# Kernel optimization log

Hardware: AMD Instinct MI355X
Metric: run time of the kernel (lower is better)

Reference implementation:

```python
import jax, jax.numpy as jnp
import numpy as np

N_NODES = 100000
N_EDGES = 1600000
N_GRAPHS = 1000
IN_DIM, HID, OUT = 100, 128, 2


def setup_inputs() -> dict:
    key = jax.random.key(0)
    ks = jax.random.split(key, 9)
    x = jax.random.normal(ks[0], (N_NODES, IN_DIM), dtype=jnp.float32)
    edge_index = jax.random.randint(ks[1], (2, N_EDGES), 0, N_NODES, dtype=jnp.int64 if jax.config.jax_enable_x64 else jnp.int32)
    batch = jnp.sort(jax.random.randint(ks[2], (N_NODES,), 0, N_GRAPHS))
    W1 = jax.random.normal(ks[3], (IN_DIM, HID), dtype=jnp.float32) / np.sqrt(IN_DIM)
    b1 = jax.random.normal(ks[4], (HID,), dtype=jnp.float32) * 0.01
    W2 = jax.random.normal(ks[5], (HID, HID), dtype=jnp.float32) / np.sqrt(HID)
    b2 = jax.random.normal(ks[6], (HID,), dtype=jnp.float32) * 0.01
    Wfc = jax.random.normal(ks[7], (HID, OUT), dtype=jnp.float32) / np.sqrt(HID)
    bfc = jax.random.normal(ks[8], (OUT,), dtype=jnp.float32) * 0.01
    return {"x": x, "edge_index": edge_index, "batch": batch, "num_graphs": N_GRAPHS,
            "W1": W1, "b1": b1, "W2": W2, "b2": b2, "Wfc": Wfc, "bfc": bfc}


def reference(x, edge_index, batch, num_graphs, W1, b1, W2, b2, Wfc, bfc):
    n = x.shape[0]
    loop = jnp.arange(n, dtype=edge_index.dtype)
    # GCNConv default: add self loops, then symmetric normalization
    src = jnp.concatenate([edge_index[0], loop])  # [E+N]
    dst = jnp.concatenate([edge_index[1], loop])
    deg = jax.ops.segment_sum(jnp.ones_like(dst, dtype=x.dtype), dst, num_segments=n)  # in-degree incl self-loop
    dinv = jnp.where(deg > 0, jax.lax.rsqrt(deg), 0.0)
    norm = (dinv[src] * dinv[dst])[:, None]  # [E+N,1]

    def gcn_conv(h, W, b):
        h = h @ W                                # transform-first (small feat dim)
        msg = h[src] * norm                      # gather + scale  [E+N, F]
        agg = jax.ops.segment_sum(msg, dst, num_segments=n)  # scatter-add
        return agg + b

    h = jax.nn.relu(gcn_conv(x, W1, b1))
    h = jax.nn.relu(gcn_conv(h, W2, b2))

    # global_mean_pool over graphs
    sums = jax.ops.segment_sum(h, batch, num_segments=num_graphs)
    cnts = jax.ops.segment_sum(jnp.ones((n,), dtype=h.dtype), batch, num_segments=num_graphs)
    pooled = sums / jnp.maximum(cnts, 1.0)[:, None]
    # dropout is identity at inference
    return pooled @ Wfc + bfc
```

## Files before the change

kernel.cpp:

```cpp
#include <hip/hip_runtime.h>


#define GCN_GRAPHS 1000
#define CSR_CAP 64
#define BUCKET_CAP 4608
#define BIN_TILE 8192
#define POOL_CHUNKS 4

typedef short bf16x8 __attribute__((ext_vector_type(8)));
typedef float f32x4 __attribute__((ext_vector_type(4)));
typedef float f32x2 __attribute__((ext_vector_type(2)));

__device__ __forceinline__ unsigned short f2bf(float x) {
  unsigned u = __float_as_uint(x);
  return (unsigned short)((u + 0x7fff + ((u >> 16) & 1)) >> 16);
}
__device__ __forceinline__ f32x2 fp8x2_f32(unsigned short u) {
  return __builtin_amdgcn_cvt_pk_f32_fp8((int)(unsigned)u, false);
}
__device__ __forceinline__ unsigned char f32_fp8(float v) {
  return (unsigned char)(__builtin_amdgcn_cvt_pk_fp8_f32(v, v, 0, false) & 0xff);
}

__global__ __launch_bounds__(256) void setup_kernel(
    const float* __restrict__ W1, const float* __restrict__ W2,
    unsigned short* __restrict__ Wf1, unsigned short* __restrict__ Wf2,
    int* __restrict__ gcursor, int nbk, const int* __restrict__ batch,
    const float* __restrict__ bfc, float* __restrict__ out,
    float* __restrict__ invcnt, int* __restrict__ gstart,
    unsigned char* __restrict__ hs1, unsigned char* __restrict__ hs2,
    int N, int G) {
  int t = blockIdx.x * 256 + threadIdx.x;
  if (t < nbk) gcursor[t] = t * BUCKET_CAP;
  if (t < 32) {
    ((unsigned*)(hs1 + ((size_t)N << 7)))[t] = 0u;
    ((unsigned*)(hs2 + ((size_t)N << 7)))[t] = 0u;
  }
  if (t <= G) {
    int lo = 0, hi = N;
    while (lo < hi) { int mid = (lo + hi) >> 1; if (batch[mid] < t) lo = mid + 1; else hi = mid; }
    gstart[t] = lo;
    if (t < G) {
      int s = lo;
      hi = N;
      while (lo < hi) { int mid = (lo + hi) >> 1; if (batch[mid] < t + 1) lo = mid + 1; else hi = mid; }
      int cnt = lo - s;
      invcnt[t] = (cnt > 0) ? 1.f / (float)cnt : 0.f;
      out[2 * t + 0] = bfc[0];
      out[2 * t + 1] = bfc[1];
    }
  }
  for (int o = t; o < 16384; o += 4096) {
    int L = (o >> 3) & 63, j = o & 7;
    int tnq = o >> 9;
    int kq = tnq >> 3, tn = tnq & 7;
    int k = kq * 32 + (L >> 4) * 8 + j;
    int n = tn * 16 + (L & 15);
    Wf1[o] = (k < 100) ? f2bf(W1[k * 128 + n]) : (unsigned short)0;
    Wf2[o] = f2bf(W2[k * 128 + n]);
  }
}

__global__ __launch_bounds__(512) void bin_kernel(
    const int* __restrict__ src, const int* __restrict__ dst,
    int* __restrict__ gcursor, int* __restrict__ bucketbuf, int E, int nbk) {
  __shared__ int hist[512];
  __shared__ int off[512];
  __shared__ int gbase[512];
  __shared__ int lcur[512];
  __shared__ int wsum[8];
  __shared__ int stage[BIN_TILE];
  __shared__ int gofs[BIN_TILE];
  const int tid = threadIdx.x;
  const int lane = tid & 63, wv = tid >> 6;
  const int tile0 = blockIdx.x * BIN_TILE;
  int cnt = E - tile0;
  if (cnt > BIN_TILE) cnt = BIN_TILE;

  hist[tid] = 0;
  __syncthreads();
  for (int i = tid; i < cnt; i += 512) {
    int b = dst[tile0 + i] >> 8;
    atomicAdd(&hist[b], 1);
  }
  __syncthreads();
  int v = hist[tid];
  int inc = v;
#pragma unroll
  for (int s = 1; s < 64; s <<= 1) {
    int u = __shfl_up(inc, s);
    if (lane >= s) inc += u;
  }
  if (lane == 63) wsum[wv] = inc;
  __syncthreads();
  if (wv == 0 && lane < 8) {
    int p = wsum[lane];
#pragma unroll
    for (int s = 1; s < 8; s <<= 1) {
      int u = __shfl_up(p, s);
      if (lane >= s) p += u;
    }
    wsum[lane] = p;
  }
  __syncthreads();
  int excl = (wv ? wsum[wv - 1] : 0) + inc - v;
  off[tid] = excl;
  if (tid < nbk && v > 0)
    gbase[tid] = atomicAdd(&gcursor[tid], v);
  lcur[tid] = 0;
  __syncthreads();
  for (int i = tid; i < cnt; i += 512) {
    int d = dst[tile0 + i];
    int s = src[tile0 + i];
    int b = d >> 8;
    int r = atomicAdd(&lcur[b], 1);
    int pos = off[b] + r;
    stage[pos] = s | ((d & 255) << 17);
    int ga = gbase[b] + r;
    gofs[pos] = (ga < (b + 1) * BUCKET_CAP) ? ga : -1;
  }
  __syncthreads();
  for (int j = tid; j < cnt; j += 512) {
    int a = gofs[j];
    if (a >= 0) bucketbuf[a] = stage[j];
  }
}

__global__ __launch_bounds__(256) void build_kernel(
    const int* __restrict__ gcursor, const int* __restrict__ bucketbuf,
    int* __restrict__ csr, int* __restrict__ deg, int N) {
  __shared__ int lcnt[256];
  __shared__ int lcsr[256 * CSR_CAP];
  const int tid = threadIdx.x;
  const int b = blockIdx.x;
  const int base = b * BUCKET_CAP;
  int cnt = gcursor[b] - base;
  if (cnt > BUCKET_CAP) cnt = BUCKET_CAP;
  lcnt[tid] = 0;
  __syncthreads();
  for (int i = tid; i < cnt; i += 256) {
    int val = bucketbuf[base + i];
    int ld = val >> 17, s = val & 0x1FFFF;
    int r = atomicAdd(&lcnt[ld], 1);
    if (r < CSR_CAP) lcsr[ld * CSR_CAP + r] = s << 7;
  }
  __syncthreads();
  const int node0 = b << 8;
  int nb = N - node0;
  if (nb > 256) nb = 256;
  const uint4* ls = (const uint4*)lcsr;
  uint4* gd = (uint4*)(csr + (size_t)node0 * CSR_CAP);
  const int nq = nb * (CSR_CAP / 4);
  for (int j = tid; j < nq; j += 256) gd[j] = ls[j];
  if (tid < nb) deg[node0 + tid] = lcnt[tid];
}

__global__ __launch_bounds__(256) void gemm_mfma_f32(
    const float* __restrict__ A, const unsigned short* __restrict__ Wfrag,
    const int* __restrict__ deg, unsigned char* __restrict__ hs, int M) {
  __shared__ unsigned short As[128 * 128];
  __shared__ unsigned short Bs[128 * 128];
  const int tid = threadIdx.x;
  const int m0 = blockIdx.x * 128;

  {
    const uint4* sp = (const uint4*)Wfrag;
    uint4* dp = (uint4*)Bs;
#pragma unroll
    for (int u = 0; u < 8; ++u) dp[u * 256 + tid] = sp[u * 256 + tid];
  }
#pragma unroll
  for (int p = 0; p < 8; ++p) {
    int q = p * 256 + tid;
    int row = q >> 4;
    int c = q & 15;
    int rowg = m0 + row;
    int tm = row >> 4, mm = row & 15;
    int kq = c >> 2, quad = c & 3;
    unsigned short* ldst = As + (((tm * 4 + kq) * 64 + quad * 16 + mm) << 3);
    unsigned short tmp[8];
#pragma unroll
    for (int u = 0; u < 4; ++u) {
      int k = c * 8 + u * 2;
      float2 v = make_float2(0.f, 0.f);
      if (rowg < M && k < 100) v = *(const float2*)(A + (size_t)rowg * 100 + k);
      tmp[u * 2] = f2bf(v.x);
      tmp[u * 2 + 1] = f2bf(v.y);
    }
    *(uint4*)ldst = *(const uint4*)tmp;
  }
  __syncthreads();

  const int w = tid >> 6, lane = tid & 63;
  f32x4 acc[2][8];
#pragma unroll
  for (int r = 0; r < 2; ++r)
#pragma unroll
    for (int tn = 0; tn < 8; ++tn) acc[r][tn] = (f32x4){0.f, 0.f, 0.f, 0.f};

#pragma unroll
  for (int kq = 0; kq < 4; ++kq) {
    bf16x8 a0 = *(const bf16x8*)(As + ((((w * 2 + 0) * 4 + kq) * 64 + lane) << 3));
    bf16x8 a1 = *(const bf16x8*)(As + ((((w * 2 + 1) * 4 + kq) * 64 + lane) << 3));
#pragma unroll
    for (int tn = 0; tn < 8; ++tn) {
      bf16x8 b = *(const bf16x8*)(Bs + (((kq * 8 + tn) * 64 + lane) << 3));
      acc[0][tn] = __builtin_amdgcn_mfma_f32_16x16x32_bf16(a0, b, acc[0][tn], 0, 0, 0);
      acc[1][tn] = __builtin_amdgcn_mfma_f32_16x16x32_bf16(a1, b, acc[1][tn], 0, 0, 0);
    }
  }

  const int colb = lane & 15;
  const int rq = lane >> 4;
#pragma unroll
  for (int r = 0; r < 2; ++r) {
#pragma unroll
    for (int i = 0; i < 4; ++i) {
      int row = m0 + (w * 2 + r) * 16 + rq * 4 + i;
      if (row < M) {
        float dv = rsqrtf((float)deg[row] + 1.f);
        unsigned char* op = hs + (size_t)row * 128 + colb;
#pragma unroll
        for (int tn = 0; tn < 8; ++tn) op[tn * 16] = f32_fp8(acc[r][tn][i] * dv);
      }
    }
  }
}

__device__ __forceinline__ void gather_core4(
    const unsigned char* __restrict__ hs, const int* __restrict__ csr,
    int nodeQ, bool valid, int cnt, int mx, int Nshift, int qsel, int ql,
    float a[8]) {
  const unsigned qloff = (unsigned)(ql << 3);
  unsigned selfOff = (valid ? ((unsigned)nodeQ << 7) : (unsigned)Nshift) + qloff;
  uint2 su = *(const uint2*)(hs + selfOff);
  {
    f32x2 l0 = fp8x2_f32((unsigned short)su.x);
    f32x2 h0 = __builtin_amdgcn_cvt_pk_f32_fp8((int)su.x, true);
    f32x2 l1 = fp8x2_f32((unsigned short)su.y);
    f32x2 h1 = __builtin_amdgcn_cvt_pk_f32_fp8((int)su.y, true);
    a[0] = l0.x; a[1] = l0.y; a[2] = h0.x; a[3] = h0.y;
    a[4] = l1.x; a[5] = l1.y; a[6] = h1.x; a[7] = h1.y;
  }
  auto acc1 = [&](uint2 u) {
    f32x2 l0 = fp8x2_f32((unsigned short)u.x);
    f32x2 h0 = __builtin_amdgcn_cvt_pk_f32_fp8((int)u.x, true);
    f32x2 l1 = fp8x2_f32((unsigned short)u.y);
    f32x2 h1 = __builtin_amdgcn_cvt_pk_f32_fp8((int)u.y, true);
    a[0] += l0.x; a[1] += l0.y; a[2] += h0.x; a[3] += h0.y;
    a[4] += l1.x; a[5] += l1.y; a[6] += h1.x; a[7] += h1.y;
  };
  const int cbase = (valid ? nodeQ : 0) * CSR_CAP + ql;
#pragma unroll
  for (int j = 0; j < 4; ++j) {
    const int jb = j * 16;
    if (mx > jb) {
      int idx = (jb + ql < cnt) ? __builtin_nontemporal_load(csr + cbase + jb)
                                : Nshift;
      int lim = mx - jb;
      if (lim > 16) lim = 16;
      int s = 0;
      for (; s + 4 <= lim; s += 4) {
        int o0 = __builtin_amdgcn_ds_bpermute(qsel + ((s + 0) << 2), idx);
        int o1 = __builtin_amdgcn_ds_bpermute(qsel + ((s + 1) << 2), idx);
        int o2 = __builtin_amdgcn_ds_bpermute(qsel + ((s + 2) << 2), idx);
        int o3 = __builtin_amdgcn_ds_bpermute(qsel + ((s + 3) << 2), idx);
        uint2 u0 = *(const uint2*)(hs + ((unsigned)o0 + qloff));
        uint2 u1 = *(const uint2*)(hs + ((unsigned)o1 + qloff));
        uint2 u2 = *(const uint2*)(hs + ((unsigned)o2 + qloff));
        uint2 u3 = *(const uint2*)(hs + ((unsigned)o3 + qloff));
        acc1(u0); acc1(u1); acc1(u2); acc1(u3);
      }
      for (; s < lim; ++s) {
        int o0 = __builtin_amdgcn_ds_bpermute(qsel + (s << 2), idx);
        uint2 u0 = *(const uint2*)(hs + ((unsigned)o0 + qloff));
        acc1(u0);
      }
    }
  }
}

__global__ __launch_bounds__(512) void gemm2_fused(
    const unsigned char* __restrict__ hs1, const unsigned short* __restrict__ Wfrag,
    const int* __restrict__ deg, const int* __restrict__ csr,
    const float* __restrict__ b1, unsigned char* __restrict__ hs2, int M, int N) {
  __shared__ unsigned short As[128 * 128];
  __shared__ unsigned short Bs[128 * 128];
  const int tid = threadIdx.x;
  const int m0 = blockIdx.x * 128;
  const int wv = tid >> 6, lane = tid & 63;
  const int q = lane >> 4, ql = lane & 15;
  const int qsel = (lane & 48) << 2;
  const int Nshift = N << 7;

  {
    const uint4* sp = (const uint4*)Wfrag;
    uint4* dp = (uint4*)Bs;
#pragma unroll
    for (int u = 0; u < 4; ++u) dp[u * 512 + tid] = sp[u * 512 + tid];
  }

  const int fql = ql << 3;
  float4 bb0 = *(const float4*)(b1 + fql);
  float4 bb1 = *(const float4*)(b1 + fql + 4);
#pragma unroll
  for (int t = 0; t < 4; ++t) {
    const int row = t * 32 + wv * 4 + q;
    const int nodeQ = m0 + row;
    const bool valid = nodeQ < M;
    int dg = valid ? deg[nodeQ] : 0;
    int cnt = dg < CSR_CAP ? dg : CSR_CAP;
    int m = cnt;
    m = max(m, __shfl_xor(m, 16));
    m = max(m, __shfl_xor(m, 32));
    const int mx = __builtin_amdgcn_readfirstlane(m);

    float a[8];
    gather_core4(hs1, csr, nodeQ, valid, cnt, mx, Nshift, qsel, ql, a);

    float dv = rsqrtf((float)dg + 1.f);
    unsigned short h[8];
    if (valid) {
      h[0] = f2bf(fmaxf(fmaf(dv, a[0], bb0.x), 0.f));
      h[1] = f2bf(fmaxf(fmaf(dv, a[1], bb0.y), 0.f));
      h[2] = f2bf(fmaxf(fmaf(dv, a[2], bb0.z), 0.f));
      h[3] = f2bf(fmaxf(fmaf(dv, a[3], bb0.w), 0.f));
      h[4] = f2bf(fmaxf(fmaf(dv, a[4], bb1.x), 0.f));
      h[5] = f2bf(fmaxf(fmaf(dv, a[5], bb1.y), 0.f));
      h[6] = f2bf(fmaxf(fmaf(dv, a[6], bb1.z), 0.f));
      h[7] = f2bf(fmaxf(fmaf(dv, a[7], bb1.w), 0.f));
    } else {
#pragma unroll
      for (int k = 0; k < 8; ++k) h[k] = 0;
    }
    unsigned short* ldst =
        As + ((((row >> 4) * 4 + (ql >> 2)) * 64 + (ql & 3) * 16 + (row & 15)) << 3);
    *(uint4*)ldst = *(const uint4*)h;
  }
  __syncthreads();

  f32x4 acc[8];
#pragma unroll
  for (int tn = 0; tn < 8; ++tn) acc[tn] = (f32x4){0.f, 0.f, 0.f, 0.f};
#pragma unroll
  for (int kq = 0; kq < 4; ++kq) {
    bf16x8 av = *(const bf16x8*)(As + (((wv * 4 + kq) * 64 + lane) << 3));
#pragma unroll
    for (int tn = 0; tn < 8; ++tn) {
      bf16x8 b = *(const bf16x8*)(Bs + (((kq * 8 + tn) * 64 + lane) << 3));
      acc[tn] = __builtin_amdgcn_mfma_f32_16x16x32_bf16(av, b, acc[tn], 0, 0, 0);
    }
  }

  const int colb = lane & 15;
  const int rq = lane >> 4;
#pragma unroll
  for (int i = 0; i < 4; ++i) {
    int row = m0 + wv * 16 + rq * 4 + i;
    if (row < M) {
      float dv = rsqrtf((float)deg[row] + 1.f);
      unsigned char* op = hs2 + (size_t)row * 128 + colb;
#pragma unroll
      for (int tn = 0; tn < 8; ++tn) op[tn * 16] = f32_fp8(acc[tn][i] * dv);
    }
  }
}

__global__ __launch_bounds__(256) void gatherpool_kernel(
    const unsigned char* __restrict__ hs, const int* __restrict__ deg,
    const int* __restrict__ csr, const float* __restrict__ b2,
    const int* __restrict__ gstart, const float* __restrict__ Wfc,
    const float* __restrict__ invcnt, float* __restrict__ out, int N) {
  __shared__ float part[4][128];
  const int g = blockIdx.x / POOL_CHUNKS;
  const int chunk = blockIdx.x % POOL_CHUNKS;
  const int tid = threadIdx.x, lane = tid & 63, wv = tid >> 6;
  const int q = lane >> 4, ql = lane & 15;
  const int qsel = (lane & 48) << 2;
  const int s = gstart[g], e = gstart[g + 1];
  const int Nshift = N << 7;
  const int f = ql << 3;
  float4 bb0 = *(const float4*)(b2 + f);
  float4 bb1 = *(const float4*)(b2 + f + 4);
  float p[8];
#pragma unroll
  for (int k = 0; k < 8; ++k) p[k] = 0.f;

  for (int d = s + (chunk * 4 + wv) * 4; d < e; d += 4 * 4 * POOL_CHUNKS) {
    const int nodeQ = d + q;
    const bool valid = nodeQ < e;
    int dg = valid ? deg[nodeQ] : 0;
    int cnt = dg < CSR_CAP ? dg : CSR_CAP;
    int m = cnt;
    m = max(m, __shfl_xor(m, 16));
    m = max(m, __shfl_xor(m, 32));
    const int mx = __builtin_amdgcn_readfirstlane(m);

    float a[8];
    gather_core4(hs, csr, nodeQ, valid, cnt, mx, Nshift, qsel, ql, a);

    float dv = rsqrtf((float)dg + 1.f);
    if (valid) {
      p[0] += fmaxf(fmaf(dv, a[0], bb0.x), 0.f);
      p[1] += fmaxf(fmaf(dv, a[1], bb0.y), 0.f);
      p[2] += fmaxf(fmaf(dv, a[2], bb0.z), 0.f);
      p[3] += fmaxf(fmaf(dv, a[3], bb0.w), 0.f);
      p[4] += fmaxf(fmaf(dv, a[4], bb1.x), 0.f);
      p[5] += fmaxf(fmaf(dv, a[5], bb1.y), 0.f);
      p[6] += fmaxf(fmaf(dv, a[6], bb1.z), 0.f);
      p[7] += fmaxf(fmaf(dv, a[7], bb1.w), 0.f);
    }
  }
#pragma unroll
  for (int k = 0; k < 8; ++k) {
    p[k] += __shfl_xor(p[k], 16);
    p[k] += __shfl_xor(p[k], 32);
  }
  if (q == 0) {
#pragma unroll
    for (int k = 0; k < 8; ++k) part[wv][f + k] = p[k];
  }
  __syncthreads();
  if (wv == 0) {
    int f2 = lane * 2;
    float ax = part[0][f2] + part[1][f2] + part[2][f2] + part[3][f2];
    float ay = part[0][f2 + 1] + part[1][f2 + 1] + part[2][f2 + 1] + part[3][f2 + 1];
    float ic = invcnt[g];
    float mx = ax * ic, my = ay * ic;
    float s0 = mx * Wfc[f2 * 2 + 0] + my * Wfc[f2 * 2 + 2];
    float s1 = mx * Wfc[f2 * 2 + 1] + my * Wfc[f2 * 2 + 3];
#pragma unroll
    for (int off = 32; off > 0; off >>= 1) {
      s0 += __shfl_down(s0, off);
      s1 += __shfl_down(s1, off);
    }
    if (lane == 0) {
      atomicAdd(&out[2 * g + 0], s0);
      atomicAdd(&out[2 * g + 1], s1);
    }
  }
}

extern "C" void kernel_launch(void* const* d_in, const int* in_sizes, int n_in,
                              void* d_out, int out_size, void* d_ws, size_t ws_size,
                              hipStream_t stream) {
  const float* x   = (const float*)d_in[0];
  const int*   ei  = (const int*)d_in[1];
  const int*   bat = (const int*)d_in[2];
  const float* W1  = (const float*)d_in[4];
  const float* b1  = (const float*)d_in[5];
  const float* W2  = (const float*)d_in[6];
  const float* b2  = (const float*)d_in[7];
  const float* Wfc = (const float*)d_in[8];
  const float* bfc = (const float*)d_in[9];

  const int N = in_sizes[2];
  const int E = in_sizes[1] / 2;
  const int G = GCN_GRAPHS;
  const int* src = ei;
  const int* dst = ei + E;
  const int nbk = (N + 255) >> 8;

  char* w = (char*)d_ws;
  auto carve = [&](size_t bytes) {
    void* p = (void*)w;
    w += (bytes + 15) & ~(size_t)15;
    return p;
  };
  int* deg       = (int*)carve((size_t)N * 4);
  int* gcursor   = (int*)carve((size_t)nbk * 4);
  float* invcnt  = (float*)carve((size_t)G * 4);
  int* gstart    = (int*)carve((size_t)(G + 1) * 4);
  unsigned short* Wf1 = (unsigned short*)carve(16384 * 2);
  unsigned short* Wf2 = (unsigned short*)carve(16384 * 2);
  int* bucketbuf = (int*)carve((size_t)nbk * BUCKET_CAP * 4);
  int* csr       = (int*)carve((size_t)N * CSR_CAP * 4);
  unsigned char* bufA = (unsigned char*)carve((size_t)(N + 1) * 128);
  unsigned char* bufC = (unsigned char*)carve((size_t)(N + 1) * 128);
  (void)ws_size; (void)n_in; (void)out_size;

  setup_kernel<<<16, 256, 0, stream>>>(W1, W2, Wf1, Wf2, gcursor, nbk, bat, bfc,
                                       (float*)d_out, invcnt, gstart, bufA, bufC, N, G);
  bin_kernel<<<(E + BIN_TILE - 1) / BIN_TILE, 512, 0, stream>>>(src, dst, gcursor,
                                                                bucketbuf, E, nbk);
  build_kernel<<<nbk, 256, 0, stream>>>(gcursor, bucketbuf, csr, deg, N);

  const int gemmBlocks = (N + 127) / 128;

  gemm_mfma_f32<<<gemmBlocks, 256, 0, stream>>>(x, Wf1, deg, bufA, N);

  gemm2_fused<<<gemmBlocks, 512, 0, stream>>>(bufA, Wf2, deg, csr, b1, bufC, N, N);

  gatherpool_kernel<<<G * POOL_CHUNKS, 256, 0, stream>>>(bufC, deg, csr, b2, gstart,
                                                         Wfc, invcnt, (float*)d_out, N);
}
```

Measured before the change: 269.4 us.

## Split fp8 feature tables into four 32-byte slabs and gather 16 nodes per wave

The fp8 hidden-feature arrays are split into four column slabs of 32 bytes per node, so each wave gathers 16 nodes at a time with 4 lanes per node, looping over the slabs. Neighbor indices are preloaded into registers once and reused across all four slabs. In the fused second GEMM the A operand now stays in registers instead of going through shared memory. The pooling kernel uses fewer chunks and reduces across nodes with shuffles. This trades wider per-lane gathers for a smaller per-slab working set that may cache better, at the cost of four passes over the index list and more registers.

```diff
diff --git a/kernel.cpp b/kernel.cpp
--- a/kernel.cpp
+++ b/kernel.cpp
@@ -5,7 +5,7 @@
 #define CSR_CAP 64
 #define BUCKET_CAP 4608
 #define BIN_TILE 8192
-#define POOL_CHUNKS 4
+#define POOL_CHUNKS 2
 
 typedef short bf16x8 __attribute__((ext_vector_type(8)));
 typedef float f32x4 __attribute__((ext_vector_type(4)));
@@ -21,6 +21,57 @@
 __device__ __forceinline__ unsigned char f32_fp8(float v) {
   return (unsigned char)(__builtin_amdgcn_cvt_pk_fp8_f32(v, v, 0, false) & 0xff);
 }
+
+#define ACC8(U)                                                              \
+  {                                                                          \
+    f32x2 l0 = fp8x2_f32((unsigned short)(U).x);                             \
+    f32x2 h0 = __builtin_amdgcn_cvt_pk_f32_fp8((int)(U).x, true);            \
+    f32x2 l1 = fp8x2_f32((unsigned short)(U).y);                             \
+    f32x2 h1 = __builtin_amdgcn_cvt_pk_f32_fp8((int)(U).y, true);            \
+    a0 += l0.x; a1 += l0.y; a2 += h0.x; a3 += h0.y;                          \
+    a4 += l1.x; a5 += l1.y; a6 += h1.x; a7 += h1.y;                          \
+  }
+#define GPROC4(REG)                                                          \
+  {                                                                          \
+    int o0 = __builtin_amdgcn_ds_bpermute(qsel, REG);                        \
+    int o1 = __builtin_amdgcn_ds_bpermute(qsel + 64, REG);                   \
+    int o2 = __builtin_amdgcn_ds_bpermute(qsel + 128, REG);                  \
+    int o3 = __builtin_amdgcn_ds_bpermute(qsel + 192, REG);                  \
+    uint2 u0 = *(const uint2*)(hsS + (unsigned)o0 + oloff);                  \
+    uint2 u1 = *(const uint2*)(hsS + (unsigned)o1 + oloff);                  \
+    uint2 u2 = *(const uint2*)(hsS + (unsigned)o2 + oloff);                  \
+    uint2 u3 = *(const uint2*)(hsS + (unsigned)o3 + oloff);                  \
+    ACC8(u0); ACC8(u1); ACC8(u2); ACC8(u3);                                  \
+  }
+#define GBLK(B, RA, RB, RC, RD)                                              \
+  if (mx > (B) * 16) {                                                       \
+    GPROC4(RA);                                                              \
+    if (mx > (B) * 16 + 4) GPROC4(RB);                                       \
+    if (mx > (B) * 16 + 8) GPROC4(RC);                                       \
+    if (mx > (B) * 16 + 12) GPROC4(RD);                                      \
+  }
+#define LDSLOT(S)                                                            \
+  ({ int _s = (S) + ol;                                                      \
+     int _v = __builtin_nontemporal_load(csr + cbase + _s);                  \
+     (_s < cnt) ? _v : Nshift; })
+#define GLD(B, RA, RB, RC, RD)                                               \
+  if (mx > (B) * 16) {                                                       \
+    RA = LDSLOT((B) * 16 + 0);                                               \
+    RB = LDSLOT((B) * 16 + 4);                                               \
+    RC = LDSLOT((B) * 16 + 8);                                               \
+    RD = LDSLOT((B) * 16 + 12);                                              \
+  }
+#define GSELF()                                                              \
+  float a0, a1, a2, a3, a4, a5, a6, a7;                                      \
+  {                                                                          \
+    uint2 su = *(const uint2*)(hsS + selfOff + oloff);                       \
+    f32x2 l0 = fp8x2_f32((unsigned short)su.x);                              \
+    f32x2 h0 = __builtin_amdgcn_cvt_pk_f32_fp8((int)su.x, true);             \
+    f32x2 l1 = fp8x2_f32((unsigned short)su.y);                              \
+    f32x2 h1 = __builtin_amdgcn_cvt_pk_f32_fp8((int)su.y, true);             \
+    a0 = l0.x; a1 = l0.y; a2 = h0.x; a3 = h0.y;                              \
+    a4 = l1.x; a5 = l1.y; a6 = h1.x; a7 = h1.y;                              \
+  }
 
 __global__ __launch_bounds__(256) void setup_kernel(
     const float* __restrict__ W1, const float* __restrict__ W2,
@@ -31,10 +82,11 @@
     unsigned char* __restrict__ hs1, unsigned char* __restrict__ hs2,
     int N, int G) {
   int t = blockIdx.x * 256 + threadIdx.x;
+  const size_t SS = (size_t)(N + 1) * 32;
   if (t < nbk) gcursor[t] = t * BUCKET_CAP;
   if (t < 32) {
-    ((unsigned*)(hs1 + ((size_t)N << 7)))[t] = 0u;
-    ((unsigned*)(hs2 + ((size_t)N << 7)))[t] = 0u;
+    ((unsigned*)(hs1 + (size_t)(t >> 3) * SS + ((size_t)N << 5)))[t & 7] = 0u;
+    ((unsigned*)(hs2 + (size_t)(t >> 3) * SS + ((size_t)N << 5)))[t & 7] = 0u;
   }
   if (t <= G) {
     int lo = 0, hi = N;
@@ -142,7 +194,7 @@
     int val = bucketbuf[base + i];
     int ld = val >> 17, s = val & 0x1FFFF;
     int r = atomicAdd(&lcnt[ld], 1);
-    if (r < CSR_CAP) lcsr[ld * CSR_CAP + r] = s << 7;
+    if (r < CSR_CAP) lcsr[ld * CSR_CAP + r] = s << 5;
   }
   __syncthreads();
   const int node0 = b << 8;
@@ -162,6 +214,7 @@
   __shared__ unsigned short Bs[128 * 128];
   const int tid = threadIdx.x;
   const int m0 = blockIdx.x * 128;
+  const size_t SS = (size_t)(M + 1) * 32;
 
   {
     const uint4* sp = (const uint4*)Wfrag;
@@ -219,62 +272,10 @@
       int row = m0 + (w * 2 + r) * 16 + rq * 4 + i;
       if (row < M) {
         float dv = rsqrtf((float)deg[row] + 1.f);
-        unsigned char* op = hs + (size_t)row * 128 + colb;
-#pragma unroll
-        for (int tn = 0; tn < 8; ++tn) op[tn * 16] = f32_fp8(acc[r][tn][i] * dv);
-      }
-    }
-  }
-}
-
-__device__ __forceinline__ void gather_core4(
-    const unsigned char* __restrict__ hs, const int* __restrict__ csr,
-    int nodeQ, bool valid, int cnt, int mx, int Nshift, int qsel, int ql,
-    float a[8]) {
-  const unsigned qloff = (unsigned)(ql << 3);
-  unsigned selfOff = (valid ? ((unsigned)nodeQ << 7) : (unsigned)Nshift) + qloff;
-  uint2 su = *(const uint2*)(hs + selfOff);
-  {
-    f32x2 l0 = fp8x2_f32((unsigned short)su.x);
-    f32x2 h0 = __builtin_amdgcn_cvt_pk_f32_fp8((int)su.x, true);
-    f32x2 l1 = fp8x2_f32((unsigned short)su.y);
-    f32x2 h1 = __builtin_amdgcn_cvt_pk_f32_fp8((int)su.y, true);
-    a[0] = l0.x; a[1] = l0.y; a[2] = h0.x; a[3] = h0.y;
-    a[4] = l1.x; a[5] = l1.y; a[6] = h1.x; a[7] = h1.y;
-  }
-  auto acc1 = [&](uint2 u) {
-    f32x2 l0 = fp8x2_f32((unsigned short)u.x);
-    f32x2 h0 = __builtin_amdgcn_cvt_pk_f32_fp8((int)u.x, true);
-    f32x2 l1 = fp8x2_f32((unsigned short)u.y);
-    f32x2 h1 = __builtin_amdgcn_cvt_pk_f32_fp8((int)u.y, true);
-    a[0] += l0.x; a[1] += l0.y; a[2] += h0.x; a[3] += h0.y;
-    a[4] += l1.x; a[5] += l1.y; a[6] += h1.x; a[7] += h1.y;
-  };
-  const int cbase = (valid ? nodeQ : 0) * CSR_CAP + ql;
-#pragma unroll
-  for (int j = 0; j < 4; ++j) {
-    const int jb = j * 16;
-    if (mx > jb) {
-      int idx = (jb + ql < cnt) ? __builtin_nontemporal_load(csr + cbase + jb)
-                                : Nshift;
-      int lim = mx - jb;
-      if (lim > 16) lim = 16;
-      int s = 0;
-      for (; s + 4 <= lim; s += 4) {
-        int o0 = __builtin_amdgcn_ds_bpermute(qsel + ((s + 0) << 2), idx);
-        int o1 = __builtin_amdgcn_ds_bpermute(qsel + ((s + 1) << 2), idx);
-        int o2 = __builtin_amdgcn_ds_bpermute(qsel + ((s + 2) << 2), idx);
-        int o3 = __builtin_amdgcn_ds_bpermute(qsel + ((s + 3) << 2), idx);
-        uint2 u0 = *(const uint2*)(hs + ((unsigned)o0 + qloff));
-        uint2 u1 = *(const uint2*)(hs + ((unsigned)o1 + qloff));
-        uint2 u2 = *(const uint2*)(hs + ((unsigned)o2 + qloff));
-        uint2 u3 = *(const uint2*)(hs + ((unsigned)o3 + qloff));
-        acc1(u0); acc1(u1); acc1(u2); acc1(u3);
-      }
-      for (; s < lim; ++s) {
-        int o0 = __builtin_amdgcn_ds_bpermute(qsel + (s << 2), idx);
-        uint2 u0 = *(const uint2*)(hs + ((unsigned)o0 + qloff));
-        acc1(u0);
+        unsigned char* op = hs + (size_t)row * 32 + colb;
+#pragma unroll
+        for (int tn = 0; tn < 8; ++tn)
+          op[(size_t)(tn >> 1) * SS + (tn & 1) * 16] = f32_fp8(acc[r][tn][i] * dv);
       }
     }
   }
@@ -284,14 +285,15 @@
     const unsigned char* __restrict__ hs1, const unsigned short* __restrict__ Wfrag,
     const int* __restrict__ deg, const int* __restrict__ csr,
     const float* __restrict__ b1, unsigned char* __restrict__ hs2, int M, int N) {
-  __shared__ unsigned short As[128 * 128];
   __shared__ unsigned short Bs[128 * 128];
   const int tid = threadIdx.x;
   const int m0 = blockIdx.x * 128;
   const int wv = tid >> 6, lane = tid & 63;
-  const int q = lane >> 4, ql = lane & 15;
-  const int qsel = (lane & 48) << 2;
-  const int Nshift = N << 7;
+  const int nl = lane & 15, ol = lane >> 4;
+  const int qsel = nl << 2;
+  const unsigned oloff = (unsigned)(ol << 3);
+  const size_t SS = (size_t)(N + 1) * 32;
+  const int Nshift = N << 5;
 
   {
     const uint4* sp = (const uint4*)Wfrag;
@@ -300,42 +302,50 @@
     for (int u = 0; u < 4; ++u) dp[u * 512 + tid] = sp[u * 512 + tid];
   }
 
-  const int fql = ql << 3;
-  float4 bb0 = *(const float4*)(b1 + fql);
-  float4 bb1 = *(const float4*)(b1 + fql + 4);
-#pragma unroll
-  for (int t = 0; t < 4; ++t) {
-    const int row = t * 32 + wv * 4 + q;
-    const int nodeQ = m0 + row;
-    const bool valid = nodeQ < M;
-    int dg = valid ? deg[nodeQ] : 0;
-    int cnt = dg < CSR_CAP ? dg : CSR_CAP;
-    int m = cnt;
-    m = max(m, __shfl_xor(m, 16));
-    m = max(m, __shfl_xor(m, 32));
-    const int mx = __builtin_amdgcn_readfirstlane(m);
-
-    float a[8];
-    gather_core4(hs1, csr, nodeQ, valid, cnt, mx, Nshift, qsel, ql, a);
-
-    float dv = rsqrtf((float)dg + 1.f);
+  const int nodeQ = m0 + wv * 16 + nl;
+  const bool valid = nodeQ < M;
+  int dg = valid ? deg[nodeQ] : 0;
+  int cnt = dg < CSR_CAP ? dg : CSR_CAP;
+  int m = cnt;
+  m = max(m, __shfl_xor(m, 1));
+  m = max(m, __shfl_xor(m, 2));
+  m = max(m, __shfl_xor(m, 4));
+  m = max(m, __shfl_xor(m, 8));
+  const int mx = __builtin_amdgcn_readfirstlane(m);
+  const int cbase = (valid ? nodeQ : 0) * CSR_CAP;
+  int i0a = Nshift, i0b = Nshift, i0c = Nshift, i0d = Nshift;
+  int i1a = Nshift, i1b = Nshift, i1c = Nshift, i1d = Nshift;
+  int i2a = Nshift, i2b = Nshift, i2c = Nshift, i2d = Nshift;
+  int i3a = Nshift, i3b = Nshift, i3c = Nshift, i3d = Nshift;
+  GLD(0, i0a, i0b, i0c, i0d)
+  GLD(1, i1a, i1b, i1c, i1d)
+  GLD(2, i2a, i2b, i2c, i2d)
+  GLD(3, i3a, i3b, i3c, i3d)
+  const float dv = rsqrtf((float)dg + 1.f);
+  const unsigned selfOff = valid ? ((unsigned)nodeQ << 5) : (unsigned)Nshift;
+
+  bf16x8 av[4];
+#pragma unroll
+  for (int s4 = 0; s4 < 4; ++s4) {
+    const unsigned char* hsS = hs1 + (size_t)s4 * SS;
+    GSELF()
+    GBLK(0, i0a, i0b, i0c, i0d)
+    GBLK(1, i1a, i1b, i1c, i1d)
+    GBLK(2, i2a, i2b, i2c, i2d)
+    GBLK(3, i3a, i3b, i3c, i3d)
+    const float* bp = b1 + ((s4 * 4 + ol) << 3);
+    float4 bb0 = *(const float4*)bp;
+    float4 bb1 = *(const float4*)(bp + 4);
     unsigned short h[8];
-    if (valid) {
-      h[0] = f2bf(fmaxf(fmaf(dv, a[0], bb0.x), 0.f));
-      h[1] = f2bf(fmaxf(fmaf(dv, a[1], bb0.y), 0.f));
-      h[2] = f2bf(fmaxf(fmaf(dv, a[2], bb0.z), 0.f));
-      h[3] = f2bf(fmaxf(fmaf(dv, a[3], bb0.w), 0.f));
-      h[4] = f2bf(fmaxf(fmaf(dv, a[4], bb1.x), 0.f));
-      h[5] = f2bf(fmaxf(fmaf(dv, a[5], bb1.y), 0.f));
-      h[6] = f2bf(fmaxf(fmaf(dv, a[6], bb1.z), 0.f));
-      h[7] = f2bf(fmaxf(fmaf(dv, a[7], bb1.w), 0.f));
-    } else {
-#pragma unroll
-      for (int k = 0; k < 8; ++k) h[k] = 0;
-    }
-    unsigned short* ldst =
-        As + ((((row >> 4) * 4 + (ql >> 2)) * 64 + (ql & 3) * 16 + (row & 15)) << 3);
-    *(uint4*)ldst = *(const uint4*)h;
+    h[0] = valid ? f2bf(fmaxf(fmaf(dv, a0, bb0.x), 0.f)) : (unsigned short)0;
+    h[1] = valid ? f2bf(fmaxf(fmaf(dv, a1, bb0.y), 0.f)) : (unsigned short)0;
+    h[2] = valid ? f2bf(fmaxf(fmaf(dv, a2, bb0.z), 0.f)) : (unsigned short)0;
+    h[3] = valid ? f2bf(fmaxf(fmaf(dv, a3, bb0.w), 0.f)) : (unsigned short)0;
+    h[4] = valid ? f2bf(fmaxf(fmaf(dv, a4, bb1.x), 0.f)) : (unsigned short)0;
+    h[5] = valid ? f2bf(fmaxf(fmaf(dv, a5, bb1.y), 0.f)) : (unsigned short)0;
+    h[6] = valid ? f2bf(fmaxf(fmaf(dv, a6, bb1.z), 0.f)) : (unsigned short)0;
+    h[7] = valid ? f2bf(fmaxf(fmaf(dv, a7, bb1.w), 0.f)) : (unsigned short)0;
+    av[s4] = *(const bf16x8*)h;
   }
   __syncthreads();
 
@@ -344,11 +354,10 @@
   for (int tn = 0; tn < 8; ++tn) acc[tn] = (f32x4){0.f, 0.f, 0.f, 0.f};
 #pragma unroll
   for (int kq = 0; kq < 4; ++kq) {
-    bf16x8 av = *(const bf16x8*)(As + (((wv * 4 + kq) * 64 + lane) << 3));
 #pragma unroll
     for (int tn = 0; tn < 8; ++tn) {
       bf16x8 b = *(const bf16x8*)(Bs + (((kq * 8 + tn) * 64 + lane) << 3));
-      acc[tn] = __builtin_amdgcn_mfma_f32_16x16x32_bf16(av, b, acc[tn], 0, 0, 0);
+      acc[tn] = __builtin_amdgcn_mfma_f32_16x16x32_bf16(av[kq], b, acc[tn], 0, 0, 0);
     }
   }
 
@@ -358,10 +367,11 @@
   for (int i = 0; i < 4; ++i) {
     int row = m0 + wv * 16 + rq * 4 + i;
     if (row < M) {
-      float dv = rsqrtf((float)deg[row] + 1.f);
-      unsigned char* op = hs2 + (size_t)row * 128 + colb;
-#pragma unroll
-      for (int tn = 0; tn < 8; ++tn) op[tn * 16] = f32_fp8(acc[tn][i] * dv);
+      float dv2 = rsqrtf((float)deg[row] + 1.f);
+      unsigned char* op = hs2 + (size_t)row * 32 + colb;
+#pragma unroll
+      for (int tn = 0; tn < 8; ++tn)
+        op[(size_t)(tn >> 1) * SS + (tn & 1) * 16] = f32_fp8(acc[tn][i] * dv2);
     }
   }
 }
@@ -375,50 +385,71 @@
   const int g = blockIdx.x / POOL_CHUNKS;
   const int chunk = blockIdx.x % POOL_CHUNKS;
   const int tid = threadIdx.x, lane = tid & 63, wv = tid >> 6;
-  const int q = lane >> 4, ql = lane & 15;
-  const int qsel = (lane & 48) << 2;
-  const int s = gstart[g], e = gstart[g + 1];
-  const int Nshift = N << 7;
-  const int f = ql << 3;
-  float4 bb0 = *(const float4*)(b2 + f);
-  float4 bb1 = *(const float4*)(b2 + f + 4);
-  float p[8];
-#pragma unroll
-  for (int k = 0; k < 8; ++k) p[k] = 0.f;
-
-  for (int d = s + (chunk * 4 + wv) * 4; d < e; d += 4 * 4 * POOL_CHUNKS) {
-    const int nodeQ = d + q;
+  const int nl = lane & 15, ol = lane >> 4;
+  const int qsel = nl << 2;
+  const unsigned oloff = (unsigned)(ol << 3);
+  const int sg = gstart[g], e = gstart[g + 1];
+  const size_t SS = (size_t)(N + 1) * 32;
+  const int Nshift = N << 5;
+  ((float*)part)[tid] = 0.f;
+  ((float*)part)[tid + 256] = 0.f;
+  __syncthreads();
+
+  for (int d0 = sg + (chunk * 4 + wv) * 16; d0 < e; d0 += 16 * 4 * POOL_CHUNKS) {
+    const int nodeQ = d0 + nl;
     const bool valid = nodeQ < e;
     int dg = valid ? deg[nodeQ] : 0;
     int cnt = dg < CSR_CAP ? dg : CSR_CAP;
     int m = cnt;
-    m = max(m, __shfl_xor(m, 16));
-    m = max(m, __shfl_xor(m, 32));
+    m = max(m, __shfl_xor(m, 1));
+    m = max(m, __shfl_xor(m, 2));
+    m = max(m, __shfl_xor(m, 4));
+    m = max(m, __shfl_xor(m, 8));
     const int mx = __builtin_amdgcn_readfirstlane(m);
-
-    float a[8];
-    gather_core4(hs, csr, nodeQ, valid, cnt, mx, Nshift, qsel, ql, a);
-
-    float dv = rsqrtf((float)dg + 1.f);
-    if (valid) {
-      p[0] += fmaxf(fmaf(dv, a[0], bb0.x), 0.f);
-      p[1] += fmaxf(fmaf(dv, a[1], bb0.y), 0.f);
-      p[2] += fmaxf(fmaf(dv, a[2], bb0.z), 0.f);
-      p[3] += fmaxf(fmaf(dv, a[3], bb0.w), 0.f);
-      p[4] += fmaxf(fmaf(dv, a[4], bb1.x), 0.f);
-      p[5] += fmaxf(fmaf(dv, a[5], bb1.y), 0.f);
-      p[6] += fmaxf(fmaf(dv, a[6], bb1.z), 0.f);
-      p[7] += fmaxf(fmaf(dv, a[7], bb1.w), 0.f);
-    }
-  }
-#pragma unroll
-  for (int k = 0; k < 8; ++k) {
-    p[k] += __shfl_xor(p[k], 16);
-    p[k] += __shfl_xor(p[k], 32);
-  }
-  if (q == 0) {
-#pragma unroll
-    for (int k = 0; k < 8; ++k) part[wv][f + k] = p[k];
+    const int cbase = (valid ? nodeQ : 0) * CSR_CAP;
+    int i0a = Nshift, i0b = Nshift, i0c = Nshift, i0d = Nshift;
+    int i1a = Nshift, i1b = Nshift, i1c = Nshift, i1d = Nshift;
+    int i2a = Nshift, i2b = Nshift, i2c = Nshift, i2d = Nshift;
+    int i3a = Nshift, i3b = Nshift, i3c = Nshift, i3d = Nshift;
+    GLD(0, i0a, i0b, i0c, i0d)
+    GLD(1, i1a, i1b, i1c, i1d)
+    GLD(2, i2a, i2b, i2c, i2d)
+    GLD(3, i3a, i3b, i3c, i3d)
+    const float dv = rsqrtf((float)dg + 1.f);
+    const unsigned selfOff = valid ? ((unsigned)nodeQ << 5) : (unsigned)Nshift;
+
+#pragma unroll
+    for (int s4 = 0; s4 < 4; ++s4) {
+      const unsigned char* hsS = hs + (size_t)s4 * SS;
+      GSELF()
+      GBLK(0, i0a, i0b, i0c, i0d)
+      GBLK(1, i1a, i1b, i1c, i1d)
+      GBLK(2, i2a, i2b, i2c, i2d)
+      GBLK(3, i3a, i3b, i3c, i3d)
+      const float* bp = b2 + ((s4 * 4 + ol) << 3);
+      float4 bb0 = *(const float4*)bp;
+      float4 bb1 = *(const float4*)(bp + 4);
+      float h0 = valid ? fmaxf(fmaf(dv, a0, bb0.x), 0.f) : 0.f;
+      float h1 = valid ? fmaxf(fmaf(dv, a1, bb0.y), 0.f) : 0.f;
+      float h2 = valid ? fmaxf(fmaf(dv, a2, bb0.z), 0.f) : 0.f;
+      float h3 = valid ? fmaxf(fmaf(dv, a3, bb0.w), 0.f) : 0.f;
+      float h4 = valid ? fmaxf(fmaf(dv, a4, bb1.x), 0.f) : 0.f;
+      float h5 = valid ? fmaxf(fmaf(dv, a5, bb1.y), 0.f) : 0.f;
+      float h6 = valid ? fmaxf(fmaf(dv, a6, bb1.z), 0.f) : 0.f;
+      float h7 = valid ? fmaxf(fmaf(dv, a7, bb1.w), 0.f) : 0.f;
+#pragma unroll
+      for (int st = 1; st <= 8; st <<= 1) {
+        h0 += __shfl_xor(h0, st); h1 += __shfl_xor(h1, st);
+        h2 += __shfl_xor(h2, st); h3 += __shfl_xor(h3, st);
+        h4 += __shfl_xor(h4, st); h5 += __shfl_xor(h5, st);
+        h6 += __shfl_xor(h6, st); h7 += __shfl_xor(h7, st);
+      }
+      if (nl == 0) {
+        float* pr = &part[wv][s4 * 32 + ol * 8];
+        pr[0] += h0; pr[1] += h1; pr[2] += h2; pr[3] += h3;
+        pr[4] += h4; pr[5] += h5; pr[6] += h6; pr[7] += h7;
+      }
+    }
   }
   __syncthreads();
   if (wv == 0) {
@@ -426,9 +457,9 @@
     float ax = part[0][f2] + part[1][f2] + part[2][f2] + part[3][f2];
     float ay = part[0][f2 + 1] + part[1][f2 + 1] + part[2][f2 + 1] + part[3][f2 + 1];
     float ic = invcnt[g];
-    float mx = ax * ic, my = ay * ic;
-    float s0 = mx * Wfc[f2 * 2 + 0] + my * Wfc[f2 * 2 + 2];
-    float s1 = mx * Wfc[f2 * 2 + 1] + my * Wfc[f2 * 2 + 3];
+    float mx2 = ax * ic, my = ay * ic;
+    float s0 = mx2 * Wfc[f2 * 2 + 0] + my * Wfc[f2 * 2 + 2];
+    float s1 = mx2 * Wfc[f2 * 2 + 1] + my * Wfc[f2 * 2 + 3];
 #pragma unroll
     for (int off = 32; off > 0; off >>= 1) {
       s0 += __shfl_down(s0, off);
```

After: 335.7 us. +24.6%, slower.

## Fuse setup into binning kernel and CSR build into first GEMM launch

Applied to the files above, without the earlier changes.

Setup work (graph boundary search, weight fragment packing, output init) now runs in extra blocks of the binning kernel. The CSR build now shares a launch with the first GEMM, with the two selected by block index. Node degree is computed with global atomics during binning, and bucket cursors become relative offsets cleared by memsets. This removes two kernel launches and their serialization gaps, but adds 1.6M scattered global atomics plus two memset operations.

```diff
diff --git a/kernel.cpp b/kernel.cpp
--- a/kernel.cpp
+++ b/kernel.cpp
@@ -22,48 +22,48 @@
   return (unsigned char)(__builtin_amdgcn_cvt_pk_fp8_f32(v, v, 0, false) & 0xff);
 }
 
-__global__ __launch_bounds__(256) void setup_kernel(
+__global__ __launch_bounds__(512) void bin_setup_kernel(
+    const int* __restrict__ src, const int* __restrict__ dst,
+    int* __restrict__ gcursor, int* __restrict__ bucketbuf, int E, int nbk,
+    int* __restrict__ deg, int binBlocks,
     const float* __restrict__ W1, const float* __restrict__ W2,
     unsigned short* __restrict__ Wf1, unsigned short* __restrict__ Wf2,
-    int* __restrict__ gcursor, int nbk, const int* __restrict__ batch,
-    const float* __restrict__ bfc, float* __restrict__ out,
-    float* __restrict__ invcnt, int* __restrict__ gstart,
-    unsigned char* __restrict__ hs1, unsigned char* __restrict__ hs2,
-    int N, int G) {
-  int t = blockIdx.x * 256 + threadIdx.x;
-  if (t < nbk) gcursor[t] = t * BUCKET_CAP;
-  if (t < 32) {
-    ((unsigned*)(hs1 + ((size_t)N << 7)))[t] = 0u;
-    ((unsigned*)(hs2 + ((size_t)N << 7)))[t] = 0u;
-  }
-  if (t <= G) {
-    int lo = 0, hi = N;
-    while (lo < hi) { int mid = (lo + hi) >> 1; if (batch[mid] < t) lo = mid + 1; else hi = mid; }
-    gstart[t] = lo;
-    if (t < G) {
-      int s = lo;
-      hi = N;
-      while (lo < hi) { int mid = (lo + hi) >> 1; if (batch[mid] < t + 1) lo = mid + 1; else hi = mid; }
-      int cnt = lo - s;
-      invcnt[t] = (cnt > 0) ? 1.f / (float)cnt : 0.f;
-      out[2 * t + 0] = bfc[0];
-      out[2 * t + 1] = bfc[1];
-    }
-  }
-  for (int o = t; o < 16384; o += 4096) {
-    int L = (o >> 3) & 63, j = o & 7;
-    int tnq = o >> 9;
-    int kq = tnq >> 3, tn = tnq & 7;
-    int k = kq * 32 + (L >> 4) * 8 + j;
-    int n = tn * 16 + (L & 15);
-    Wf1[o] = (k < 100) ? f2bf(W1[k * 128 + n]) : (unsigned short)0;
-    Wf2[o] = f2bf(W2[k * 128 + n]);
-  }
-}
-
-__global__ __launch_bounds__(512) void bin_kernel(
-    const int* __restrict__ src, const int* __restrict__ dst,
-    int* __restrict__ gcursor, int* __restrict__ bucketbuf, int E, int nbk) {
+    const int* __restrict__ batch, const float* __restrict__ bfc,
+    float* __restrict__ out, float* __restrict__ invcnt,
+    int* __restrict__ gstart, unsigned char* __restrict__ hs1,
+    unsigned char* __restrict__ hs2, int N, int G) {
+  const int tid = threadIdx.x;
+  if ((int)blockIdx.x >= binBlocks) {
+    int t = ((int)blockIdx.x - binBlocks) * 512 + tid;
+    if (t < 32) {
+      ((unsigned*)(hs1 + ((size_t)N << 7)))[t] = 0u;
+      ((unsigned*)(hs2 + ((size_t)N << 7)))[t] = 0u;
+    }
+    if (t <= G) {
+      int lo = 0, hi = N;
+      while (lo < hi) { int mid = (lo + hi) >> 1; if (batch[mid] < t) lo = mid + 1; else hi = mid; }
+      gstart[t] = lo;
+      if (t < G) {
+        int s = lo;
+        hi = N;
+        while (lo < hi) { int mid = (lo + hi) >> 1; if (batch[mid] < t + 1) lo = mid + 1; else hi = mid; }
+        int cnt = lo - s;
+        invcnt[t] = (cnt > 0) ? 1.f / (float)cnt : 0.f;
+        out[2 * t + 0] = bfc[0];
+        out[2 * t + 1] = bfc[1];
+      }
+    }
+    for (int o = t; o < 16384; o += 4096) {
+      int L = (o >> 3) & 63, j = o & 7;
+      int tnq = o >> 9;
+      int kq = tnq >> 3, tn = tnq & 7;
+      int k = kq * 32 + (L >> 4) * 8 + j;
+      int n = tn * 16 + (L & 15);
+      Wf1[o] = (k < 100) ? f2bf(W1[k * 128 + n]) : (unsigned short)0;
+      Wf2[o] = f2bf(W2[k * 128 + n]);
+    }
+    return;
+  }
   __shared__ int hist[512];
   __shared__ int off[512];
   __shared__ int gbase[512];
@@ -71,7 +71,6 @@
   __shared__ int wsum[8];
   __shared__ int stage[BIN_TILE];
   __shared__ int gofs[BIN_TILE];
-  const int tid = threadIdx.x;
   const int lane = tid & 63, wv = tid >> 6;
   const int tile0 = blockIdx.x * BIN_TILE;
   int cnt = E - tile0;
@@ -80,8 +79,9 @@
   hist[tid] = 0;
   __syncthreads();
   for (int i = tid; i < cnt; i += 512) {
-    int b = dst[tile0 + i] >> 8;
-    atomicAdd(&hist[b], 1);
+    int d = dst[tile0 + i];
+    atomicAdd(&hist[d >> 8], 1);
+    atomicAdd(&deg[d], 1);
   }
   __syncthreads();
   int v = hist[tid];
@@ -106,7 +106,7 @@
   int excl = (wv ? wsum[wv - 1] : 0) + inc - v;
   off[tid] = excl;
   if (tid < nbk && v > 0)
-    gbase[tid] = atomicAdd(&gcursor[tid], v);
+    gbase[tid] = tid * BUCKET_CAP + atomicAdd(&gcursor[tid], v);
   lcur[tid] = 0;
   __syncthreads();
   for (int i = tid; i < cnt; i += 512) {
@@ -126,42 +126,42 @@
   }
 }
 
-__global__ __launch_bounds__(256) void build_kernel(
+__global__ __launch_bounds__(256) void build_gemm1(
     const int* __restrict__ gcursor, const int* __restrict__ bucketbuf,
-    int* __restrict__ csr, int* __restrict__ deg, int N) {
-  __shared__ int lcnt[256];
-  __shared__ int lcsr[256 * CSR_CAP];
+    int* __restrict__ csr, const float* __restrict__ A,
+    const unsigned short* __restrict__ Wfrag, const int* __restrict__ deg,
+    unsigned char* __restrict__ hs, int M, int nbk) {
+  __shared__ int lds[16640];
   const int tid = threadIdx.x;
-  const int b = blockIdx.x;
-  const int base = b * BUCKET_CAP;
-  int cnt = gcursor[b] - base;
-  if (cnt > BUCKET_CAP) cnt = BUCKET_CAP;
-  lcnt[tid] = 0;
-  __syncthreads();
-  for (int i = tid; i < cnt; i += 256) {
-    int val = bucketbuf[base + i];
-    int ld = val >> 17, s = val & 0x1FFFF;
-    int r = atomicAdd(&lcnt[ld], 1);
-    if (r < CSR_CAP) lcsr[ld * CSR_CAP + r] = s << 7;
-  }
-  __syncthreads();
-  const int node0 = b << 8;
-  int nb = N - node0;
-  if (nb > 256) nb = 256;
-  const uint4* ls = (const uint4*)lcsr;
-  uint4* gd = (uint4*)(csr + (size_t)node0 * CSR_CAP);
-  const int nq = nb * (CSR_CAP / 4);
-  for (int j = tid; j < nq; j += 256) gd[j] = ls[j];
-  if (tid < nb) deg[node0 + tid] = lcnt[tid];
-}
-
-__global__ __launch_bounds__(256) void gemm_mfma_f32(
-    const float* __restrict__ A, const unsigned short* __restrict__ Wfrag,
-    const int* __restrict__ deg, unsigned char* __restrict__ hs, int M) {
-  __shared__ unsigned short As[128 * 128];
-  __shared__ unsigned short Bs[128 * 128];
-  const int tid = threadIdx.x;
-  const int m0 = blockIdx.x * 128;
+  if ((int)blockIdx.x < nbk) {
+    int* lcnt = lds;
+    int* lcsr = lds + 256;
+    const int b = blockIdx.x;
+    const int base = b * BUCKET_CAP;
+    int cnt = gcursor[b];
+    if (cnt > BUCKET_CAP) cnt = BUCKET_CAP;
+    lcnt[tid] = 0;
+    __syncthreads();
+    for (int i = tid; i < cnt; i += 256) {
+      int val = bucketbuf[base + i];
+      int ld = val >> 17, s = val & 0x1FFFF;
+      int r = atomicAdd(&lcnt[ld], 1);
+      if (r < CSR_CAP) lcsr[ld * CSR_CAP + r] = s << 7;
+    }
+    __syncthreads();
+    const int node0 = b << 8;
+    int nb = 256;
+    const uint4* ls = (const uint4*)lcsr;
+    uint4* gd = (uint4*)(csr + (size_t)node0 * CSR_CAP);
+    const int nq = nb * (CSR_CAP / 4);
+    for (int j = tid; j < nq; j += 256) {
+      if ((node0 + (j >> 4)) < M) gd[j] = ls[j];
+    }
+    return;
+  }
+  unsigned short* As = (unsigned short*)lds;
+  unsigned short* Bs = (unsigned short*)lds + 16384;
+  const int m0 = ((int)blockIdx.x - nbk) * 128;
 
   {
     const uint4* sp = (const uint4*)Wfrag;
@@ -479,15 +479,17 @@
   unsigned char* bufC = (unsigned char*)carve((size_t)(N + 1) * 128);
   (void)ws_size; (void)n_in; (void)out_size;
 
-  setup_kernel<<<16, 256, 0, stream>>>(W1, W2, Wf1, Wf2, gcursor, nbk, bat, bfc,
-                                       (float*)d_out, invcnt, gstart, bufA, bufC, N, G);
-  bin_kernel<<<(E + BIN_TILE - 1) / BIN_TILE, 512, 0, stream>>>(src, dst, gcursor,
-                                                                bucketbuf, E, nbk);
-  build_kernel<<<nbk, 256, 0, stream>>>(gcursor, bucketbuf, csr, deg, N);
+  hipMemsetAsync(gcursor, 0, (size_t)nbk * 4, stream);
+  hipMemsetAsync(deg, 0, (size_t)N * 4, stream);
+
+  const int binBlocks = (E + BIN_TILE - 1) / BIN_TILE;
+  bin_setup_kernel<<<binBlocks + 8, 512, 0, stream>>>(
+      src, dst, gcursor, bucketbuf, E, nbk, deg, binBlocks,
+      W1, W2, Wf1, Wf2, bat, bfc, (float*)d_out, invcnt, gstart, bufA, bufC, N, G);
 
   const int gemmBlocks = (N + 127) / 128;
-
-  gemm_mfma_f32<<<gemmBlocks, 256, 0, stream>>>(x, Wf1, deg, bufA, N);
+  build_gemm1<<<nbk + gemmBlocks, 256, 0, stream>>>(
+      gcursor, bucketbuf, csr, x, Wf1, deg, bufA, N, nbk);
 
   gemm2_fused<<<gemmBlocks, 512, 0, stream>>>(bufA, Wf2, deg, csr, b1, bufC, N, N);
 
```

After: 315.1 us. +16.9%, slower.
